# Kernel optimization log

Hardware: AMD Instinct MI355X
Metric: run time of the kernel (lower is better)

Reference implementation:

```python
import jax, jax.numpy as jnp
import numpy as np


def setup_inputs() -> dict:
    key = jax.random.key(0)
    k1, k2, k3, k4 = jax.random.split(key, 4)
    B, N, C_IN, C_OUT, K = 8, 4096, 64, 64, 16
    H = W = 64  # H * W == N
    x = jax.random.normal(k1, (B, N, C_IN), dtype=jnp.float32)
    edge_index = jax.random.randint(k2, (B, N, K), 0, N, dtype=jnp.int64)
    # 1x1 Conv2d(2*C_IN -> C_OUT) is a [C_OUT, 2*C_IN] matmul + bias
    weight = jax.random.normal(k3, (C_OUT, 2 * C_IN), dtype=jnp.float32) * 0.05
    bias = jax.random.normal(k4, (C_OUT,), dtype=jnp.float32) * 0.01
    return {"x": x, "edge_index": edge_index, "weight": weight, "bias": bias,
            "H": H, "W": W}


def reference(x, edge_index, weight, bias, H, W):
    # x: [B, N, C], edge_index: [B, N, K] with values in [0, N)
    B, N, C = x.shape
    K = edge_index.shape[-1]
    # Gather neighbor features per batch element (batched index_select)
    idx = edge_index.reshape(B, N * K, 1)                      # [B, N*K, 1]
    neighbors = jnp.take_along_axis(x, idx, axis=1)            # [B, N*K, C]
    neighbors = neighbors.reshape(B, N, K, C)                  # [B, N, K, C]
    x_central = x[:, :, None, :]                               # [B, N, 1, C]
    # edge feature: concat([x_i, x_j - x_i]) -> [B, N, K, 2C]
    edge_feat = jnp.concatenate(
        [jnp.broadcast_to(x_central, (B, N, K, C)), neighbors - x_central],
        axis=-1)
    # 1x1 conv + ReLU
    out = jax.nn.relu(jnp.einsum('bnkc,oc->bnko', edge_feat, weight) + bias)
    # max over neighbors k -> [B, N, C_out]
    out = jnp.max(out, axis=2)
    # [B, C_out, N] -> [B, C_out, H, W]
    return jnp.transpose(out, (0, 2, 1)).reshape(B, weight.shape[0], H, W)
```

## Files before the change

### kernel.cpp

```cpp
#include <hip/hip_runtime.h>
#include <stdint.h>

#define B_SZ    8
#define N_PTS   4096
#define C_IN    64
#define C_OUT   64
#define KNN     16
#define ROWS    (B_SZ * N_PTS)

typedef __attribute__((ext_vector_type(8))) short v8s;
typedef __attribute__((ext_vector_type(4))) float v4f;

__device__ inline unsigned short f2bf(float f) {
    unsigned int u = __float_as_uint(f);
    return (unsigned short)((u + 0x7FFFu + ((u >> 16) & 1u)) >> 16);
}

__device__ inline v8s pack8(float4 q0, float4 q1) {
    v8s a;
    a[0] = (short)f2bf(q0.x); a[1] = (short)f2bf(q0.y);
    a[2] = (short)f2bf(q0.z); a[3] = (short)f2bf(q0.w);
    a[4] = (short)f2bf(q1.x); a[5] = (short)f2bf(q1.y);
    a[6] = (short)f2bf(q1.z); a[7] = (short)f2bf(q1.w);
    return a;
}

#define PITCH 68

__global__ __launch_bounds__(256, 4) void proj_nbuf(
    const float* __restrict__ x,
    const float* __restrict__ w,
    unsigned short* __restrict__ nbuf)
{
    __shared__ float wl2[C_OUT][PITCH];

    const int t     = threadIdx.x;
    const int lane  = t & 63;
    const int wv    = t >> 6;
    const int rq    = wv & 1;
    const int ch    = wv >> 1;
    const int batch = blockIdx.x & 7;
    const int chunk = blockIdx.x >> 3;
    const int r0    = batch * N_PTS + chunk * 32 + rq * 16;

    const int fc   = lane & 15;
    const int koff = 8 * (lane >> 4);

    const int arow = r0 + fc;
    v8s afrag[2];
#pragma unroll
    for (int ks = 0; ks < 2; ++ks) {
        const float* xp = x + (size_t)arow * C_IN + ks * 32 + koff;
        afrag[ks] = pack8(*(const float4*)xp, *(const float4*)(xp + 4));
    }

#pragma unroll
    for (int i = 0; i < 4; ++i) {
        const int idx = i * 256 + t;
        const int col = idx >> 4;
        const int q   = (idx & 15) * 4;
        *(float4*)&wl2[col][q] = *(const float4*)(w + col * 128 + 64 + q);
    }
    __syncthreads();

    v8s bfrag[2][2];
#pragma unroll
    for (int ct = 0; ct < 2; ++ct) {
        const int col = ch * 32 + ct * 16 + fc;
#pragma unroll
        for (int ks = 0; ks < 2; ++ks) {
            const float* p = &wl2[col][ks * 32 + koff];
            bfrag[ct][ks] = pack8(*(const float4*)p, *(const float4*)(p + 4));
        }
    }

    v4f acc[2];
#pragma unroll
    for (int ct = 0; ct < 2; ++ct)
        acc[ct] = (v4f){0.f, 0.f, 0.f, 0.f};

#pragma unroll
    for (int ks = 0; ks < 2; ++ks)
#pragma unroll
        for (int ct = 0; ct < 2; ++ct)
            acc[ct] = __builtin_amdgcn_mfma_f32_16x16x32_bf16(
                afrag[ks], bfrag[ct][ks], acc[ct], 0, 0, 0);

    const int crow0 = r0 + (lane >> 4) * 4;
#pragma unroll
    for (int ct = 0; ct < 2; ++ct)
#pragma unroll
        for (int reg = 0; reg < 4; ++reg)
            nbuf[(size_t)(crow0 + reg) * C_OUT + ch * 32 + ct * 16 + fc] =
                f2bf(acc[ct][reg]);
}

__global__ __launch_bounds__(256, 4) void gather_fused(
    const float* __restrict__ x,
    const float* __restrict__ w,
    const float* __restrict__ bias,
    const int* __restrict__ eidx,
    const unsigned short* __restrict__ nbuf,
    float* __restrict__ out)
{
    __shared__ float wld[C_OUT][PITCH];
    __shared__ float sm[32][PITCH];

    const int t    = threadIdx.x;
    const int lane = t & 63;
    const int wv   = t >> 6;
    const int b    = blockIdx.x & 7;
    const int tn   = blockIdx.x >> 3;
    const int n0   = tn * 32;
    const int r0g  = b * N_PTS + n0;

    const int sub  = lane >> 3;
    const int o8   = (lane & 7) * 8;
    const int rbl  = wv * 8 + sub;
    int pidx[KNN];
    {
        const int* ep = eidx + (size_t)(r0g + rbl) * KNN;
        const int4 i0 = *(const int4*)ep;
        const int4 i1 = *(const int4*)(ep + 4);
        const int4 i2 = *(const int4*)(ep + 8);
        const int4 i3 = *(const int4*)(ep + 12);
        pidx[0]=i0.x&(N_PTS-1); pidx[1]=i0.y&(N_PTS-1); pidx[2]=i0.z&(N_PTS-1); pidx[3]=i0.w&(N_PTS-1);
        pidx[4]=i1.x&(N_PTS-1); pidx[5]=i1.y&(N_PTS-1); pidx[6]=i1.z&(N_PTS-1); pidx[7]=i1.w&(N_PTS-1);
        pidx[8]=i2.x&(N_PTS-1); pidx[9]=i2.y&(N_PTS-1); pidx[10]=i2.z&(N_PTS-1); pidx[11]=i2.w&(N_PTS-1);
        pidx[12]=i3.x&(N_PTS-1); pidx[13]=i3.y&(N_PTS-1); pidx[14]=i3.z&(N_PTS-1); pidx[15]=i3.w&(N_PTS-1);
    }

#pragma unroll
    for (int i = 0; i < 4; ++i) {
        const int idx = i * 256 + t;
        const int col = idx >> 4;
        const int q   = (idx & 15) * 4;
        const float4 w1 = *(const float4*)(w + col * 128 + q);
        const float4 w2 = *(const float4*)(w + col * 128 + 64 + q);
        *(float4*)&wld[col][q] =
            make_float4(w1.x - w2.x, w1.y - w2.y, w1.z - w2.z, w1.w - w2.w);
    }

    {
        const float4* xsrc = (const float4*)(x + (size_t)r0g * C_IN);
#pragma unroll
        for (int i = 0; i < 2; ++i) {
            const int idx = i * 256 + t;
            *(float4*)&sm[idx >> 4][(idx & 15) * 4] = xsrc[idx];
        }
    }
    __syncthreads();

    const int rq   = wv & 1;
    const int ch   = wv >> 1;
    const int rl0  = rq * 16;
    const int fc   = lane & 15;
    const int koff = 8 * (lane >> 4);

    v8s bC[2][2];
#pragma unroll
    for (int ct = 0; ct < 2; ++ct) {
        const int col = ch * 32 + ct * 16 + fc;
#pragma unroll
        for (int ks = 0; ks < 2; ++ks) {
            const float* p = &wld[col][ks * 32 + koff];
            bC[ct][ks] = pack8(*(const float4*)p, *(const float4*)(p + 4));
        }
    }

    const int rl = rl0 + fc;
    v8s af[2];
#pragma unroll
    for (int ks = 0; ks < 2; ++ks) {
        const float* xp = &sm[rl][ks * 32 + koff];
        af[ks] = pack8(*(const float4*)xp, *(const float4*)(xp + 4));
    }

    v4f acc[2];
#pragma unroll
    for (int ct = 0; ct < 2; ++ct) {
        const float bv = bias[ch * 32 + ct * 16 + fc];
        acc[ct] = (v4f){bv, bv, bv, bv};
    }
#pragma unroll
    for (int ks = 0; ks < 2; ++ks)
#pragma unroll
        for (int ct = 0; ct < 2; ++ct)
            acc[ct] = __builtin_amdgcn_mfma_f32_16x16x32_bf16(
                af[ks], bC[ct][ks], acc[ct], 0, 0, 0);

    __syncthreads();

    const int orow = rl0 + (lane >> 4) * 4;
#pragma unroll
    for (int ct = 0; ct < 2; ++ct)
#pragma unroll
        for (int reg = 0; reg < 4; ++reg)
            sm[orow + reg][ch * 32 + ct * 16 + fc] = acc[ct][reg];

    __syncthreads();

    const unsigned short* nb = nbuf + (size_t)b * N_PTS * C_OUT;

    const float4 cva = *(const float4*)&sm[rbl][o8];
    const float4 cvb = *(const float4*)&sm[rbl][o8 + 4];

    float m0 = -1e30f, m1 = -1e30f, m2 = -1e30f, m3 = -1e30f;
    float m4 = -1e30f, m5 = -1e30f, m6 = -1e30f, m7 = -1e30f;
#pragma unroll
    for (int k = 0; k < KNN; ++k) {
        const uint4 v = *(const uint4*)(nb + (size_t)pidx[k] * C_OUT + o8);
        m0 = fmaxf(m0, __uint_as_float(v.x << 16));
        m1 = fmaxf(m1, __uint_as_float(v.x & 0xffff0000u));
        m2 = fmaxf(m2, __uint_as_float(v.y << 16));
        m3 = fmaxf(m3, __uint_as_float(v.y & 0xffff0000u));
        m4 = fmaxf(m4, __uint_as_float(v.z << 16));
        m5 = fmaxf(m5, __uint_as_float(v.z & 0xffff0000u));
        m6 = fmaxf(m6, __uint_as_float(v.w << 16));
        m7 = fmaxf(m7, __uint_as_float(v.w & 0xffff0000u));
    }

    sm[rbl][o8 + 0] = fmaxf(cva.x + m0, 0.f);
    sm[rbl][o8 + 1] = fmaxf(cva.y + m1, 0.f);
    sm[rbl][o8 + 2] = fmaxf(cva.z + m2, 0.f);
    sm[rbl][o8 + 3] = fmaxf(cva.w + m3, 0.f);
    sm[rbl][o8 + 4] = fmaxf(cvb.x + m4, 0.f);
    sm[rbl][o8 + 5] = fmaxf(cvb.y + m5, 0.f);
    sm[rbl][o8 + 6] = fmaxf(cvb.z + m6, 0.f);
    sm[rbl][o8 + 7] = fmaxf(cvb.w + m7, 0.f);

    __syncthreads();

    float* ob = out + (size_t)b * C_OUT * N_PTS + n0;
    const int nn = lane & 31;
    const int oh = lane >> 5;
#pragma unroll
    for (int j = 0; j < 8; ++j) {
        const int o = wv * 16 + j * 2 + oh;
        ob[(size_t)o * N_PTS + nn] = sm[nn][o];
    }
}

extern "C" void kernel_launch(void* const* d_in, const int* in_sizes, int n_in,
                              void* d_out, int out_size, void* d_ws, size_t ws_size,
                              hipStream_t stream)
{
    const float* x    = (const float*)d_in[0];
    const int*   eidx = (const int*)d_in[1];
    const float* w    = (const float*)d_in[2];
    const float* bias = (const float*)d_in[3];
    float*       out  = (float*)d_out;

    unsigned short* nbuf = (unsigned short*)d_ws;

    proj_nbuf<<<ROWS / 32, 256, 0, stream>>>(x, w, nbuf);
    gather_fused<<<ROWS / 32, 256, 0, stream>>>(x, w, bias, eidx, nbuf, out);
}
```

Baseline: 17.07 us.

## Move central-term projection into first kernel, store fp32 center buffer

The central-point projection (x·(W1−W2)+bias) moves from the gather kernel into the projection kernel, which now computes both the center and neighbor projections from the same x fragments. The results go to a new fp32 workspace buffer. The gather kernel becomes a lean gather-max that reads this center buffer instead of reloading x and weights and running MFMAs. This removes the duplicate x read and weight prep from the gather stage and lightens that kernel. In exchange it adds an 8 MB fp32 write and read through global memory.

```diff
diff --git a/kernel.cpp b/kernel.cpp
--- a/kernel.cpp
+++ b/kernel.cpp
@@ -27,11 +27,14 @@
 
 #define PITCH 68
 
-__global__ __launch_bounds__(256, 4) void proj_nbuf(
+__global__ __launch_bounds__(256, 4) void proj_both(
     const float* __restrict__ x,
     const float* __restrict__ w,
+    const float* __restrict__ bias,
+    float* __restrict__ cbuf,
     unsigned short* __restrict__ nbuf)
 {
+    __shared__ float wld[C_OUT][PITCH];
     __shared__ float wl2[C_OUT][PITCH];
 
     const int t     = threadIdx.x;
@@ -59,51 +62,61 @@
         const int idx = i * 256 + t;
         const int col = idx >> 4;
         const int q   = (idx & 15) * 4;
-        *(float4*)&wl2[col][q] = *(const float4*)(w + col * 128 + 64 + q);
+        const float4 w1 = *(const float4*)(w + col * 128 + q);
+        const float4 w2 = *(const float4*)(w + col * 128 + 64 + q);
+        *(float4*)&wld[col][q] =
+            make_float4(w1.x - w2.x, w1.y - w2.y, w1.z - w2.z, w1.w - w2.w);
+        *(float4*)&wl2[col][q] = w2;
     }
     __syncthreads();
 
-    v8s bfrag[2][2];
+    v8s bC[2][2], bN[2][2];
 #pragma unroll
     for (int ct = 0; ct < 2; ++ct) {
         const int col = ch * 32 + ct * 16 + fc;
 #pragma unroll
         for (int ks = 0; ks < 2; ++ks) {
-            const float* p = &wl2[col][ks * 32 + koff];
-            bfrag[ct][ks] = pack8(*(const float4*)p, *(const float4*)(p + 4));
+            const float* pc = &wld[col][ks * 32 + koff];
+            const float* pn = &wl2[col][ks * 32 + koff];
+            bC[ct][ks] = pack8(*(const float4*)pc, *(const float4*)(pc + 4));
+            bN[ct][ks] = pack8(*(const float4*)pn, *(const float4*)(pn + 4));
         }
     }
 
-    v4f acc[2];
+    v4f accC[2], accN[2];
+#pragma unroll
+    for (int ct = 0; ct < 2; ++ct) {
+        const float bv = bias[ch * 32 + ct * 16 + fc];
+        accC[ct] = (v4f){bv, bv, bv, bv};
+        accN[ct] = (v4f){0.f, 0.f, 0.f, 0.f};
+    }
+#pragma unroll
+    for (int ks = 0; ks < 2; ++ks)
+#pragma unroll
+        for (int ct = 0; ct < 2; ++ct) {
+            accC[ct] = __builtin_amdgcn_mfma_f32_16x16x32_bf16(
+                afrag[ks], bC[ct][ks], accC[ct], 0, 0, 0);
+            accN[ct] = __builtin_amdgcn_mfma_f32_16x16x32_bf16(
+                afrag[ks], bN[ct][ks], accN[ct], 0, 0, 0);
+        }
+
+    const int crow0 = r0 + (lane >> 4) * 4;
 #pragma unroll
     for (int ct = 0; ct < 2; ++ct)
-        acc[ct] = (v4f){0.f, 0.f, 0.f, 0.f};
-
-#pragma unroll
-    for (int ks = 0; ks < 2; ++ks)
-#pragma unroll
-        for (int ct = 0; ct < 2; ++ct)
-            acc[ct] = __builtin_amdgcn_mfma_f32_16x16x32_bf16(
-                afrag[ks], bfrag[ct][ks], acc[ct], 0, 0, 0);
-
-    const int crow0 = r0 + (lane >> 4) * 4;
-#pragma unroll
-    for (int ct = 0; ct < 2; ++ct)
-#pragma unroll
-        for (int reg = 0; reg < 4; ++reg)
-            nbuf[(size_t)(crow0 + reg) * C_OUT + ch * 32 + ct * 16 + fc] =
-                f2bf(acc[ct][reg]);
-}
-
-__global__ __launch_bounds__(256, 4) void gather_fused(
-    const float* __restrict__ x,
-    const float* __restrict__ w,
-    const float* __restrict__ bias,
+#pragma unroll
+        for (int reg = 0; reg < 4; ++reg) {
+            const size_t off = (size_t)(crow0 + reg) * C_OUT + ch * 32 + ct * 16 + fc;
+            cbuf[off] = accC[ct][reg];
+            nbuf[off] = f2bf(accN[ct][reg]);
+        }
+}
+
+__global__ __launch_bounds__(256, 4) void gather_only(
+    const float* __restrict__ cbuf,
+    const unsigned short* __restrict__ nbuf,
     const int* __restrict__ eidx,
-    const unsigned short* __restrict__ nbuf,
     float* __restrict__ out)
 {
-    __shared__ float wld[C_OUT][PITCH];
     __shared__ float sm[32][PITCH];
 
     const int t    = threadIdx.x;
@@ -114,9 +127,10 @@
     const int n0   = tn * 32;
     const int r0g  = b * N_PTS + n0;
 
-    const int sub  = lane >> 3;
-    const int o8   = (lane & 7) * 8;
-    const int rbl  = wv * 8 + sub;
+    const int sub = lane >> 3;
+    const int o8  = (lane & 7) * 8;
+    const int rbl = wv * 8 + sub;
+
     int pidx[KNN];
     {
         const int* ep = eidx + (size_t)(r0g + rbl) * KNN;
@@ -130,81 +144,11 @@
         pidx[12]=i3.x&(N_PTS-1); pidx[13]=i3.y&(N_PTS-1); pidx[14]=i3.z&(N_PTS-1); pidx[15]=i3.w&(N_PTS-1);
     }
 
-#pragma unroll
-    for (int i = 0; i < 4; ++i) {
-        const int idx = i * 256 + t;
-        const int col = idx >> 4;
-        const int q   = (idx & 15) * 4;
-        const float4 w1 = *(const float4*)(w + col * 128 + q);
-        const float4 w2 = *(const float4*)(w + col * 128 + 64 + q);
-        *(float4*)&wld[col][q] =
-            make_float4(w1.x - w2.x, w1.y - w2.y, w1.z - w2.z, w1.w - w2.w);
-    }
-
-    {
-        const float4* xsrc = (const float4*)(x + (size_t)r0g * C_IN);
-#pragma unroll
-        for (int i = 0; i < 2; ++i) {
-            const int idx = i * 256 + t;
-            *(float4*)&sm[idx >> 4][(idx & 15) * 4] = xsrc[idx];
-        }
-    }
-    __syncthreads();
-
-    const int rq   = wv & 1;
-    const int ch   = wv >> 1;
-    const int rl0  = rq * 16;
-    const int fc   = lane & 15;
-    const int koff = 8 * (lane >> 4);
-
-    v8s bC[2][2];
-#pragma unroll
-    for (int ct = 0; ct < 2; ++ct) {
-        const int col = ch * 32 + ct * 16 + fc;
-#pragma unroll
-        for (int ks = 0; ks < 2; ++ks) {
-            const float* p = &wld[col][ks * 32 + koff];
-            bC[ct][ks] = pack8(*(const float4*)p, *(const float4*)(p + 4));
-        }
-    }
-
-    const int rl = rl0 + fc;
-    v8s af[2];
-#pragma unroll
-    for (int ks = 0; ks < 2; ++ks) {
-        const float* xp = &sm[rl][ks * 32 + koff];
-        af[ks] = pack8(*(const float4*)xp, *(const float4*)(xp + 4));
-    }
-
-    v4f acc[2];
-#pragma unroll
-    for (int ct = 0; ct < 2; ++ct) {
-        const float bv = bias[ch * 32 + ct * 16 + fc];
-        acc[ct] = (v4f){bv, bv, bv, bv};
-    }
-#pragma unroll
-    for (int ks = 0; ks < 2; ++ks)
-#pragma unroll
-        for (int ct = 0; ct < 2; ++ct)
-            acc[ct] = __builtin_amdgcn_mfma_f32_16x16x32_bf16(
-                af[ks], bC[ct][ks], acc[ct], 0, 0, 0);
-
-    __syncthreads();
-
-    const int orow = rl0 + (lane >> 4) * 4;
-#pragma unroll
-    for (int ct = 0; ct < 2; ++ct)
-#pragma unroll
-        for (int reg = 0; reg < 4; ++reg)
-            sm[orow + reg][ch * 32 + ct * 16 + fc] = acc[ct][reg];
-
-    __syncthreads();
+    const float* cp = cbuf + (size_t)(r0g + rbl) * C_OUT + o8;
+    const float4 cva = *(const float4*)cp;
+    const float4 cvb = *(const float4*)(cp + 4);
 
     const unsigned short* nb = nbuf + (size_t)b * N_PTS * C_OUT;
-
-    const float4 cva = *(const float4*)&sm[rbl][o8];
-    const float4 cvb = *(const float4*)&sm[rbl][o8 + 4];
-
     float m0 = -1e30f, m1 = -1e30f, m2 = -1e30f, m3 = -1e30f;
     float m4 = -1e30f, m5 = -1e30f, m6 = -1e30f, m7 = -1e30f;
 #pragma unroll
@@ -252,7 +196,8 @@
     float*       out  = (float*)d_out;
 
     unsigned short* nbuf = (unsigned short*)d_ws;
-
-    proj_nbuf<<<ROWS / 32, 256, 0, stream>>>(x, w, nbuf);
-    gather_fused<<<ROWS / 32, 256, 0, stream>>>(x, w, bias, eidx, nbuf, out);
-}
+    float*          cbuf = (float*)(nbuf + (size_t)ROWS * C_OUT);
+
+    proj_both<<<ROWS / 32, 256, 0, stream>>>(x, w, bias, cbuf, nbuf);
+    gather_only<<<ROWS / 32, 256, 0, stream>>>(cbuf, nbuf, eidx, out);
+}
```

After: 17.73 us. +3.9%, slower.
